# Kernel tuning notes

Hardware: AMD Instinct MI355X
Metric: run time of the kernel (lower is better)

The kernel has to match this reference:

```python
import jax, jax.numpy as jnp
import numpy as np

HEADS = 16
KV_HEADS = 4
DIM_HEAD = 64
DIM = 1024
B, N = 2, 2048


def setup_inputs() -> dict:
    key = jax.random.key(0)
    k1, k2, k3 = jax.random.split(key, 3)
    x = jax.random.normal(k1, (B, N, DIM), dtype=jnp.float32)
    Wq = jax.random.normal(k2, (DIM, HEADS * DIM_HEAD), dtype=jnp.float32) / np.sqrt(DIM)
    Wkv = jax.random.normal(k3, (DIM, 2 * KV_HEADS * DIM_HEAD), dtype=jnp.float32) / np.sqrt(DIM)
    k_scale = jnp.ones((HEADS, 1, DIM_HEAD), dtype=jnp.float32)
    return {"x": x, "Wq": Wq, "Wkv": Wkv, "k_scale": k_scale}


def reference(x, Wq, Wkv, k_scale):
    b, n, _ = x.shape
    g = HEADS // KV_HEADS  # query heads per kv head
    scale = DIM_HEAD ** -0.5
    # fused qkv projections (no bias)
    q = (x @ Wq).reshape(b, n, HEADS, DIM_HEAD)
    kv = x @ Wkv
    k, v = jnp.split(kv, 2, axis=-1)
    k = k.reshape(b, n, KV_HEADS, DIM_HEAD).transpose(0, 2, 1, 3)  # b k n d
    v = v.reshape(b, n, KV_HEADS, DIM_HEAD).transpose(0, 2, 1, 3)  # b k n d
    # group query heads: b, kv_heads, g, n, d
    qg = q.transpose(0, 2, 1, 3).reshape(b, KV_HEADS, g, n, DIM_HEAD)
    # per-query-head k scale, applied to the group-broadcast k (qk-norm)
    ks = k_scale.reshape(KV_HEADS, g, 1, DIM_HEAD)
    kk = k[:, :, None, :, :] * ks  # b k g n d
    dots = jnp.einsum('bkgid,bkgjd->bkgij', qg, kk) * scale
    attn = jax.nn.softmax(dots, axis=-1)
    out = jnp.einsum('bkgij,bkjd->bkgid', attn, v)  # v broadcast over g
    out = out.reshape(b, HEADS, n, DIM_HEAD).transpose(0, 2, 1, 3).reshape(b, n, HEADS * DIM_HEAD)
    return out
```

## Files before the change

### kernel.cpp

```cpp
#include <hip/hip_runtime.h>
#include <stdint.h>
#include <math.h>

typedef __attribute__((ext_vector_type(8))) __bf16 bf16x8;
typedef __attribute__((ext_vector_type(4))) float f32x4;
typedef __attribute__((ext_vector_type(16))) float f32x16;

__device__ __forceinline__ uint32_t f32_to_bf16_rne(float f) {
  union { float f; uint32_t u; } v; v.f = f;
  return (v.u + 0x7FFFu + ((v.u >> 16) & 1u)) >> 16;
}

__device__ __forceinline__ uint32_t cvt_pk_bf16(float lo, float hi) {
  uint32_t r;
  asm("v_cvt_pk_bf16_f32 %0, %1, %2" : "=v"(r) : "v"(lo), "v"(hi));
  return r;
}

__device__ __forceinline__ void gld16(void* lds, const void* g) {
  __builtin_amdgcn_global_load_lds(
      (__attribute__((address_space(1))) void*)(g),
      (__attribute__((address_space(3))) void*)(lds), 16, 0, 0);
}

__device__ __forceinline__ f32x4 mfma16(bf16x8 a, bf16x8 b, f32x4 c) {
  return __builtin_amdgcn_mfma_f32_16x16x32_bf16(a, b, c, 0, 0, 0);
}
__device__ __forceinline__ f32x16 mfma32(bf16x8 a, bf16x8 b, f32x16 c) {
  return __builtin_amdgcn_mfma_f32_32x32x16_bf16(a, b, c, 0, 0, 0);
}

#define LOG2E 1.44269504088896340736f

__global__ __launch_bounds__(256) void k_convert(const float* __restrict__ x,
                                                 const float* __restrict__ wq,
                                                 const float* __restrict__ wkv,
                                                 uint16_t* __restrict__ xb,
                                                 uint16_t* __restrict__ wt) {
  __shared__ float tile[64][65];
  int blk = blockIdx.x;
  int t = threadIdx.x;
  if (blk < 2048) {
    int i = blk * 256 + t;
    const float4* xv = (const float4*)x;
    float4 a = xv[2 * i], b2 = xv[2 * i + 1];
    uint32_t w0 = f32_to_bf16_rne(a.x) | (f32_to_bf16_rne(a.y) << 16);
    uint32_t w1 = f32_to_bf16_rne(a.z) | (f32_to_bf16_rne(a.w) << 16);
    uint32_t w2 = f32_to_bf16_rne(b2.x) | (f32_to_bf16_rne(b2.y) << 16);
    uint32_t w3 = f32_to_bf16_rne(b2.z) | (f32_to_bf16_rne(b2.w) << 16);
    ((uint4*)xb)[i] = make_uint4(w0, w1, w2, w3);
  } else {
    int blk2 = blk - 2048;
    int c0 = (blk2 % 24) * 64, k0 = (blk2 / 24) * 64;
    int col = t & 63, rq = t >> 6;
#pragma unroll
    for (int rr = 0; rr < 16; rr++) {
      int r = rr * 4 + rq;
      int c = c0 + col;
      float v = (c < 1024) ? wq[(uint64_t)(k0 + r) * 1024 + c]
                           : wkv[(uint64_t)(k0 + r) * 512 + (c - 1024)];
      tile[r][col] = v;
    }
    __syncthreads();
#pragma unroll
    for (int rr = 0; rr < 16; rr++) {
      int a = rr * 4 + rq;
      wt[(uint64_t)(c0 + a) * 1024 + k0 + col] = (uint16_t)f32_to_bf16_rne(tile[col][a]);
    }
  }
}

__global__ __launch_bounds__(256, 3) void k_proj_gemm(
    const uint16_t* __restrict__ xb, const uint16_t* __restrict__ wt,
    const float* __restrict__ kscale, uint16_t* __restrict__ q_ws,
    uint16_t* __restrict__ kf_ws, uint16_t* __restrict__ vf_ws) {
  __shared__ __align__(16) uint16_t ring[4][6144];
  int t = threadIdx.x;
  int w = t >> 6, l = t & 63;
  int lq = l & 15, lg = l >> 4;
  int m0 = blockIdx.x * 128, n0 = blockIdx.y * 64;
  int wr = w >> 1, wc = w & 1;
  f32x4 acc[4][2] = {};

  auto stage = [&](int slot, int k0) {
#pragma unroll
    for (int j = 0; j < 2; j++) {
      int tt = j * 256 + t;
      int r = tt >> 2, s = tt & 3;
      int sl = s ^ ((r >> 1) & 3);
      gld16((char*)&ring[slot][0] + (j * 256 + w * 64) * 16,
            xb + (uint64_t)(m0 + r) * 1024 + k0 + sl * 8);
    }
    {
      int r = t >> 2, s = t & 3;
      int sl = s ^ ((r >> 1) & 3);
      gld16((char*)&ring[slot][4096] + (w * 64) * 16,
            wt + (uint64_t)(n0 + r) * 1024 + k0 + sl * 8);
    }
  };

  struct PFrags { bf16x8 a[4]; bf16x8 b[2]; };
  auto readFrags = [&](PFrags& F, int slot) {
    const uint16_t* As = &ring[slot][0];
    const uint16_t* Bs = &ring[slot][4096];
#pragma unroll
    for (int m = 0; m < 4; m++) {
      int r = wr * 64 + m * 16 + lq;
      int s = lg ^ ((r >> 1) & 3);
      F.a[m] = *(const bf16x8*)(As + r * 32 + s * 8);
    }
#pragma unroll
    for (int n = 0; n < 2; n++) {
      int r = wc * 32 + n * 16 + lq;
      int s = lg ^ ((r >> 1) & 3);
      F.b[n] = *(const bf16x8*)(Bs + r * 32 + s * 8);
    }
  };

  auto pbody = [&](int tt2, PFrags& C, PFrags& N) {
    int kn = (tt2 + 3) * 32;
    if (kn > 992) kn = 992;
    stage((tt2 + 3) & 3, kn);
    __builtin_amdgcn_s_setprio(1);
#pragma unroll
    for (int m = 0; m < 4; m++)
#pragma unroll
      for (int n = 0; n < 2; n++)
        acc[m][n] = mfma16(C.a[m], C.b[n], acc[m][n]);
    __builtin_amdgcn_s_setprio(0);
    int tn = tt2 + 1;
    if (tn > 31) tn = 31;
    readFrags(N, tn & 3);
    asm volatile("s_waitcnt vmcnt(3) lgkmcnt(0)" ::: "memory");
    __builtin_amdgcn_s_barrier();
  };

  stage(0, 0);
  stage(1, 32);
  stage(2, 64);
  asm volatile("s_waitcnt vmcnt(3)" ::: "memory");
  __builtin_amdgcn_s_barrier();
  PFrags FA, FB;
  readFrags(FA, 0);
  for (int sp = 0; sp < 16; ++sp) {
    pbody(2 * sp, FA, FB);
    pbody(2 * sp + 1, FB, FA);
  }

#pragma unroll
  for (int m = 0; m < 4; m++)
#pragma unroll
    for (int n = 0; n < 2; n++)
#pragma unroll
      for (int jj = 0; jj < 4; jj++) {
        int row = m0 + wr * 64 + m * 16 + 4 * lg + jj;
        int col = n0 + wc * 32 + n * 16 + lq;
        float val = acc[m][n][jj];
        int b = row >> 11, nn = row & 2047;
        if (col < 1024) {
          val *= kscale[col] * 0.125f * LOG2E;
          q_ws[((uint64_t)((b * 16 + (col >> 6)) * 2048 + nn)) * 64 + (col & 63)] =
              (uint16_t)f32_to_bf16_rne(val);
        } else if (col < 1280) {
          int kvh = (col - 1024) >> 6;
          int d = col & 63;
          int gsu = nn >> 5, lrr = nn & 31;
          int mm = d >> 4, hh = (d >> 3) & 1, el = d & 7;
          kf_ws[(uint64_t)(b * 4 + kvh) * 131072 +
                (uint64_t)((((gsu * 4 + mm) * 64) + hh * 32 + lrr) * 8 + el)] =
              (uint16_t)f32_to_bf16_rne(val);
        } else {
          int kvh = (col - 1280) >> 6;
          int d = col & 63;
          int gsu = nn >> 5, jj2 = (nn >> 4) & 1, hh = (nn >> 3) & 1, el = nn & 7;
          int dd = d >> 5, lrr = d & 31;
          vf_ws[(uint64_t)(b * 4 + kvh) * 131072 +
                (uint64_t)((((gsu * 4 + dd * 2 + jj2) * 64) + hh * 32 + lrr) * 8 + el)] =
              (uint16_t)f32_to_bf16_rne(val);
        }
      }
}

__global__ __launch_bounds__(512, 1) void k_attn(const uint16_t* __restrict__ q_ws,
                                                 const uint16_t* __restrict__ kf_ws,
                                                 const uint16_t* __restrict__ vf_ws,
                                                 float* __restrict__ out) {
  extern __shared__ __align__(16) char smem[];

  int t = threadIdx.x, w = t >> 6, l = t & 63;
  int lr = l & 31, hi = l >> 5;
  int qg = w & 3, half = w >> 2;
  int blk = blockIdx.x;
  int c = blk & 7, j = blk >> 3;
  int b = c >> 2, kvh = c & 3;
  int h = kvh * 4 + (j >> 3), qb = j & 7;

  const uint16_t* Qb = q_ws + (uint64_t)(b * 16 + h) * 2048 * 64;
  const uint16_t* Kb = kf_ws + (uint64_t)(b * 4 + kvh) * 131072;
  const uint16_t* Vb = vf_ws + (uint64_t)(b * 4 + kvh) * 131072;
  int qrow0 = qb * 256 + qg * 64;

  bf16x8 qfA[4], qfB[4];
#pragma unroll
  for (int m = 0; m < 4; m++) {
    qfA[m] = *(const bf16x8*)(Qb + (uint64_t)(qrow0 + lr) * 64 + m * 16 + hi * 8);
    qfB[m] = *(const bf16x8*)(Qb + (uint64_t)(qrow0 + 32 + lr) * 64 + m * 16 + hi * 8);
  }

  f32x16 oaccA[2] = {}, oaccB[2] = {};
  float lA = 0.f, lB = 0.f;

  const uint16_t* SbW = ((qg < 2) ? Kb : Vb) + (uint64_t)half * 65536 +
                        (uint64_t)((qg & 1) * 2) * 512 + l * 8;
  char* dstW = smem + half * 8192 + ((qg < 2) ? 0 : 4096) + (qg & 1) * 2048 + l * 16;

  auto stage = [&](int slot, int sul) {
    char* d = dstW + slot * 16384;
    const uint16_t* s = SbW + (uint64_t)sul * 2048;
    gld16(d, s);
    gld16(d + 1024, s + 512);
  };
  auto slotbase = [&](int slot) {
    return (const uint16_t*)(smem + slot * 16384 + half * 8192);
  };

  auto finish = [&](f32x16& Tc, const bf16x8* vf, f32x16* oacc, float& lsum) {
    float p[16];
#pragma unroll
    for (int e = 0; e < 16; e++) p[e] = __builtin_amdgcn_exp2f(Tc[e]);
    float sm0 = ((p[0] + p[1]) + (p[2] + p[3])) + ((p[4] + p[5]) + (p[6] + p[7]));
    float sm1 = ((p[8] + p[9]) + (p[10] + p[11])) + ((p[12] + p[13]) + (p[14] + p[15]));
    lsum += sm0 + sm1;

    bf16x8 pa[2];
#pragma unroll
    for (int jj = 0; jj < 2; jj++) {
      const float* pp = p + 8 * jj;
      uint32_t X = cvt_pk_bf16(pp[0], pp[1]);
      uint32_t Z = cvt_pk_bf16(pp[2], pp[3]);
      uint32_t Y = cvt_pk_bf16(pp[4], pp[5]);
      uint32_t W2 = cvt_pk_bf16(pp[6], pp[7]);
      asm volatile("v_permlane32_swap_b32 %0, %1" : "+v"(X), "+v"(Y));
      asm volatile("v_permlane32_swap_b32 %0, %1" : "+v"(Z), "+v"(W2));
      union { uint32_t u[4]; bf16x8 v; } pu;
      pu.u[0] = X; pu.u[1] = Z; pu.u[2] = Y; pu.u[3] = W2;
      pa[jj] = pu.v;
    }

    __builtin_amdgcn_s_setprio(1);
#pragma unroll
    for (int dd = 0; dd < 2; dd++)
#pragma unroll
      for (int jj = 0; jj < 2; jj++)
        oacc[dd] = mfma32(pa[jj], vf[dd * 2 + jj], oacc[dd]);
    __builtin_amdgcn_s_setprio(0);
  };

#pragma unroll
  for (int tt = 0; tt < 4; ++tt) stage(tt, tt);
  asm volatile("s_waitcnt vmcnt(6)" ::: "memory");
  __builtin_amdgcn_s_barrier();

  for (int su = 0; su < 32; ++su) {
    int sn = su + 4;
    if (sn > 31) sn = 31;
    stage((su + 4) % 6, sn);

    const uint16_t* base = slotbase(su % 6);
    bf16x8 kf[4];
#pragma unroll
    for (int m = 0; m < 4; m++) kf[m] = *(const bf16x8*)(base + m * 512 + l * 8);

    f32x16 Ta = {}, Tb = {};
    __builtin_amdgcn_s_setprio(1);
#pragma unroll
    for (int m = 0; m < 4; m++) Ta = mfma32(kf[m], qfA[m], Ta);
#pragma unroll
    for (int m = 0; m < 4; m++) Tb = mfma32(kf[m], qfB[m], Tb);
    __builtin_amdgcn_s_setprio(0);

    bf16x8 vf[4];
#pragma unroll
    for (int i = 0; i < 4; i++) vf[i] = *(const bf16x8*)(base + (4 + i) * 512 + l * 8);

    finish(Ta, vf, oaccA, lA);
    finish(Tb, vf, oaccB, lB);

    asm volatile("s_waitcnt vmcnt(6)" ::: "memory");
    __builtin_amdgcn_s_barrier();
  }

  lA += __shfl_xor(lA, 32);
  lB += __shfl_xor(lB, 32);

  asm volatile("s_waitcnt vmcnt(0)" ::: "memory");
  __syncthreads();

  float* exch = (float*)smem;
  float* exl = (float*)(smem + 65536);
  if (half == 1) {
#pragma unroll
    for (int sub = 0; sub < 2; sub++) {
      f32x16* oacc = sub ? oaccB : oaccA;
#pragma unroll
      for (int r = 0; r < 16; r++) {
        int qr = (r & 3) + 8 * (r >> 2) + 4 * hi;
        exch[qg * 4096 + (sub * 32 + qr) * 64 + lr] = oacc[0][r];
        exch[qg * 4096 + (sub * 32 + qr) * 64 + 32 + lr] = oacc[1][r];
      }
    }
    if (hi == 0) {
      exl[qg * 64 + lr] = lA;
      exl[qg * 64 + 32 + lr] = lB;
    }
  }
  __syncthreads();
  if (half == 0) {
    lA += exl[qg * 64 + lr];
    lB += exl[qg * 64 + 32 + lr];
    float invA = 1.0f / lA, invB = 1.0f / lB;
#pragma unroll
    for (int sub = 0; sub < 2; sub++) {
      f32x16* oacc = sub ? oaccB : oaccA;
      float inv = sub ? invB : invA;
#pragma unroll
      for (int r = 0; r < 16; r++) {
        int qr = (r & 3) + 8 * (r >> 2) + 4 * hi;
        float iv = __shfl(inv, qr);
        float o0 = oacc[0][r] + exch[qg * 4096 + (sub * 32 + qr) * 64 + lr];
        float o1 = oacc[1][r] + exch[qg * 4096 + (sub * 32 + qr) * 64 + 32 + lr];
        float* orow =
            out + (uint64_t)(b * 2048 + qrow0 + sub * 32 + qr) * 1024 + h * 64 + lr;
        orow[0] = o0 * iv;
        orow[32] = o1 * iv;
      }
    }
  }
}

extern "C" void kernel_launch(void* const* d_in, const int* in_sizes, int n_in,
                              void* d_out, int out_size, void* d_ws, size_t ws_size,
                              hipStream_t stream) {
  const float* x = (const float*)d_in[0];
  const float* wq = (const float*)d_in[1];
  const float* wkv = (const float*)d_in[2];
  const float* kscale = (const float*)d_in[3];
  float* out = (float*)d_out;
  char* ws = (char*)d_ws;
  uint16_t* xb = (uint16_t*)(ws);
  uint16_t* wt = (uint16_t*)(ws + (8ull << 20));
  uint16_t* q_ws = (uint16_t*)(ws + (11ull << 20));
  uint16_t* kf_ws = (uint16_t*)(ws + (19ull << 20));
  uint16_t* vf_ws = (uint16_t*)(ws + (21ull << 20));

  static bool attr_set = false;
  if (!attr_set) {
    (void)hipFuncSetAttribute((const void*)k_attn,
                              hipFuncAttributeMaxDynamicSharedMemorySize, 98304);
    attr_set = true;
  }

  k_convert<<<2432, 256, 0, stream>>>(x, wq, wkv, xb, wt);
  k_proj_gemm<<<dim3(32, 24), 256, 0, stream>>>(xb, wt, kscale, q_ws, kf_ws, vf_ws);
  k_attn<<<256, 512, 98304, stream>>>(q_ws, kf_ws, vf_ws, out);
}
```

Baseline: 76.78 us.

## Deepen GEMM K-tile to 64 and process two KV tiles per attention iteration

The projection GEMM moves from a 4-slot ring of 32-wide K tiles to a 3-slot ring of 64-wide tiles with an 8-way XOR swizzle. This halves the number of barriers but drops the register double-buffering of fragments and lowers occupancy to 2 blocks. The attention kernel grows its LDS ring from 6 to 8 slots (128KB dynamic shared memory) and handles two KV tiles per barrier. The two wave halves use different instruction orders, apparently to stagger MFMA and exp work. The larger LDS footprint and fewer waves may reduce latency hiding.

```diff
diff --git a/kernel.cpp b/kernel.cpp
--- a/kernel.cpp
+++ b/kernel.cpp
@@ -70,11 +70,11 @@
   }
 }
 
-__global__ __launch_bounds__(256, 3) void k_proj_gemm(
+__global__ __launch_bounds__(256, 2) void k_proj_gemm(
     const uint16_t* __restrict__ xb, const uint16_t* __restrict__ wt,
     const float* __restrict__ kscale, uint16_t* __restrict__ q_ws,
     uint16_t* __restrict__ kf_ws, uint16_t* __restrict__ vf_ws) {
-  __shared__ __align__(16) uint16_t ring[4][6144];
+  __shared__ __align__(16) uint16_t ring[3][12288];
   int t = threadIdx.x;
   int w = t >> 6, l = t & 63;
   int lq = l & 15, lg = l >> 4;
@@ -84,67 +84,62 @@
 
   auto stage = [&](int slot, int k0) {
 #pragma unroll
+    for (int j = 0; j < 4; j++) {
+      int c = j * 256 + t;
+      int r = c >> 3, s = c & 7;
+      int sl = s ^ (r & 7);
+      gld16((char*)&ring[slot][0] + c * 16,
+            xb + (uint64_t)(m0 + r) * 1024 + k0 + sl * 8);
+    }
+#pragma unroll
     for (int j = 0; j < 2; j++) {
-      int tt = j * 256 + t;
-      int r = tt >> 2, s = tt & 3;
-      int sl = s ^ ((r >> 1) & 3);
-      gld16((char*)&ring[slot][0] + (j * 256 + w * 64) * 16,
-            xb + (uint64_t)(m0 + r) * 1024 + k0 + sl * 8);
-    }
-    {
-      int r = t >> 2, s = t & 3;
-      int sl = s ^ ((r >> 1) & 3);
-      gld16((char*)&ring[slot][4096] + (w * 64) * 16,
+      int c = j * 256 + t;
+      int r = c >> 3, s = c & 7;
+      int sl = s ^ (r & 7);
+      gld16((char*)&ring[slot][8192] + c * 16,
             wt + (uint64_t)(n0 + r) * 1024 + k0 + sl * 8);
     }
   };
 
-  struct PFrags { bf16x8 a[4]; bf16x8 b[2]; };
-  auto readFrags = [&](PFrags& F, int slot) {
-    const uint16_t* As = &ring[slot][0];
-    const uint16_t* Bs = &ring[slot][4096];
-#pragma unroll
-    for (int m = 0; m < 4; m++) {
-      int r = wr * 64 + m * 16 + lq;
-      int s = lg ^ ((r >> 1) & 3);
-      F.a[m] = *(const bf16x8*)(As + r * 32 + s * 8);
-    }
-#pragma unroll
-    for (int n = 0; n < 2; n++) {
-      int r = wc * 32 + n * 16 + lq;
-      int s = lg ^ ((r >> 1) & 3);
-      F.b[n] = *(const bf16x8*)(Bs + r * 32 + s * 8);
-    }
-  };
-
-  auto pbody = [&](int tt2, PFrags& C, PFrags& N) {
-    int kn = (tt2 + 3) * 32;
-    if (kn > 992) kn = 992;
-    stage((tt2 + 3) & 3, kn);
+  stage(0, 0);
+  stage(1, 64);
+  asm volatile("s_waitcnt vmcnt(6)" ::: "memory");
+  __builtin_amdgcn_s_barrier();
+
+  for (int it = 0; it < 16; ++it) {
+    int tn = it + 2;
+    int kn = (tn < 16) ? tn * 64 : (tn - 3) * 64;
+    stage(tn % 3, kn);
+    asm volatile("s_waitcnt vmcnt(6)" ::: "memory");
+    __builtin_amdgcn_s_barrier();
+
+    const uint16_t* As = &ring[it % 3][0];
+    const uint16_t* Bs = &ring[it % 3][8192];
+    bf16x8 af[2][4], bfr[2][2];
+#pragma unroll
+    for (int kk = 0; kk < 2; kk++) {
+#pragma unroll
+      for (int m = 0; m < 4; m++) {
+        int r = wr * 64 + m * 16 + lq;
+        int sl = (kk * 4 + lg) ^ (r & 7);
+        af[kk][m] = *(const bf16x8*)(As + r * 64 + sl * 8);
+      }
+#pragma unroll
+      for (int n = 0; n < 2; n++) {
+        int r = wc * 32 + n * 16 + lq;
+        int sl = (kk * 4 + lg) ^ (r & 7);
+        bfr[kk][n] = *(const bf16x8*)(Bs + r * 64 + sl * 8);
+      }
+    }
     __builtin_amdgcn_s_setprio(1);
 #pragma unroll
-    for (int m = 0; m < 4; m++)
-#pragma unroll
-      for (int n = 0; n < 2; n++)
-        acc[m][n] = mfma16(C.a[m], C.b[n], acc[m][n]);
+    for (int kk = 0; kk < 2; kk++)
+#pragma unroll
+      for (int m = 0; m < 4; m++)
+#pragma unroll
+        for (int n = 0; n < 2; n++)
+          acc[m][n] = mfma16(af[kk][m], bfr[kk][n], acc[m][n]);
     __builtin_amdgcn_s_setprio(0);
-    int tn = tt2 + 1;
-    if (tn > 31) tn = 31;
-    readFrags(N, tn & 3);
-    asm volatile("s_waitcnt vmcnt(3) lgkmcnt(0)" ::: "memory");
-    __builtin_amdgcn_s_barrier();
-  };
-
-  stage(0, 0);
-  stage(1, 32);
-  stage(2, 64);
-  asm volatile("s_waitcnt vmcnt(3)" ::: "memory");
-  __builtin_amdgcn_s_barrier();
-  PFrags FA, FB;
-  readFrags(FA, 0);
-  for (int sp = 0; sp < 16; ++sp) {
-    pbody(2 * sp, FA, FB);
-    pbody(2 * sp + 1, FB, FA);
   }
 
 #pragma unroll
@@ -224,6 +219,23 @@
     return (const uint16_t*)(smem + slot * 16384 + half * 8192);
   };
 
+  auto readK = [&](bf16x8* kf, const uint16_t* base) {
+#pragma unroll
+    for (int m = 0; m < 4; m++) kf[m] = *(const bf16x8*)(base + m * 512 + l * 8);
+  };
+  auto readV = [&](bf16x8* vf, const uint16_t* base) {
+#pragma unroll
+    for (int i = 0; i < 4; i++) vf[i] = *(const bf16x8*)(base + (4 + i) * 512 + l * 8);
+  };
+  auto qk = [&](const bf16x8* kf, const bf16x8* qf) {
+    f32x16 T = {};
+    __builtin_amdgcn_s_setprio(1);
+#pragma unroll
+    for (int m = 0; m < 4; m++) T = mfma32(kf[m], qf[m], T);
+    __builtin_amdgcn_s_setprio(0);
+    return T;
+  };
+
   auto finish = [&](f32x16& Tc, const bf16x8* vf, f32x16* oacc, float& lsum) {
     float p[16];
 #pragma unroll
@@ -257,36 +269,53 @@
   };
 
 #pragma unroll
-  for (int tt = 0; tt < 4; ++tt) stage(tt, tt);
-  asm volatile("s_waitcnt vmcnt(6)" ::: "memory");
+  for (int tt = 0; tt < 6; ++tt) stage(tt, tt);
+  asm volatile("s_waitcnt vmcnt(4)" ::: "memory");
   __builtin_amdgcn_s_barrier();
 
-  for (int su = 0; su < 32; ++su) {
-    int sn = su + 4;
-    if (sn > 31) sn = 31;
-    stage((su + 4) % 6, sn);
-
-    const uint16_t* base = slotbase(su % 6);
-    bf16x8 kf[4];
-#pragma unroll
-    for (int m = 0; m < 4; m++) kf[m] = *(const bf16x8*)(base + m * 512 + l * 8);
-
-    f32x16 Ta = {}, Tb = {};
-    __builtin_amdgcn_s_setprio(1);
-#pragma unroll
-    for (int m = 0; m < 4; m++) Ta = mfma32(kf[m], qfA[m], Ta);
-#pragma unroll
-    for (int m = 0; m < 4; m++) Tb = mfma32(kf[m], qfB[m], Tb);
-    __builtin_amdgcn_s_setprio(0);
-
-    bf16x8 vf[4];
-#pragma unroll
-    for (int i = 0; i < 4; i++) vf[i] = *(const bf16x8*)(base + (4 + i) * 512 + l * 8);
-
-    finish(Ta, vf, oaccA, lA);
-    finish(Tb, vf, oaccB, lB);
-
-    asm volatile("s_waitcnt vmcnt(6)" ::: "memory");
+  for (int iv = 0; iv < 16; ++iv) {
+    int a = 2 * iv;
+    int s0 = a + 6, s1 = a + 7;
+    if (s0 > 31) s0 = 31;
+    if (s1 > 31) s1 = 31;
+    stage((a + 6) & 7, s0);
+    stage((a + 7) & 7, s1);
+
+    const uint16_t* b0 = slotbase(a & 7);
+    const uint16_t* b1 = slotbase((a + 1) & 7);
+
+    if (half == 0) {
+      bf16x8 kf[4], vf[4];
+      readK(kf, b0);
+      readV(vf, b0);
+      f32x16 Ta = qk(kf, qfA);
+      f32x16 Tb = qk(kf, qfB);
+      finish(Ta, vf, oaccA, lA);
+      finish(Tb, vf, oaccB, lB);
+      readK(kf, b1);
+      readV(vf, b1);
+      Ta = qk(kf, qfA);
+      Tb = qk(kf, qfB);
+      finish(Ta, vf, oaccA, lA);
+      finish(Tb, vf, oaccB, lB);
+    } else {
+      bf16x8 kf0[4], kf1[4];
+      readK(kf0, b0);
+      readK(kf1, b1);
+      f32x16 T0a = qk(kf0, qfA);
+      f32x16 T0b = qk(kf0, qfB);
+      f32x16 T1a = qk(kf1, qfA);
+      f32x16 T1b = qk(kf1, qfB);
+      bf16x8 vf[4];
+      readV(vf, b0);
+      finish(T0a, vf, oaccA, lA);
+      finish(T0b, vf, oaccB, lB);
+      readV(vf, b1);
+      finish(T1a, vf, oaccA, lA);
+      finish(T1b, vf, oaccB, lB);
+    }
+
+    asm volatile("s_waitcnt vmcnt(8)" ::: "memory");
     __builtin_amdgcn_s_barrier();
   }
 
@@ -356,11 +385,11 @@
   static bool attr_set = false;
   if (!attr_set) {
     (void)hipFuncSetAttribute((const void*)k_attn,
-                              hipFuncAttributeMaxDynamicSharedMemorySize, 98304);
+                              hipFuncAttributeMaxDynamicSharedMemorySize, 131072);
     attr_set = true;
   }
 
   k_convert<<<2432, 256, 0, stream>>>(x, wq, wkv, xb, wt);
   k_proj_gemm<<<dim3(32, 24), 256, 0, stream>>>(xb, wt, kscale, q_ws, kf_ws, vf_ws);
-  k_attn<<<256, 512, 98304, stream>>>(q_ws, kf_ws, vf_ws, out);
-}
+  k_attn<<<256, 512, 131072, stream>>>(q_ws, kf_ws, vf_ws, out);
+}
```

Measured after the change: 74.94 us. 1.02x faster.
